# Kernel tuning notes

Measured on AMD Instinct MI355X. Metric: run time of the kernel, lower is better.

## Reference

```python
import jax, jax.numpy as jnp
import numpy as np

B = 4096          # batch size (per-view)
D = 128           # projection dim
TEMPERATURE = 0.5
TAU_PLUS = 0.1
DROP_FN = True


def setup_inputs() -> dict:
    key = jax.random.key(0)
    k1, k2, k3, k4 = jax.random.split(key, 4)

    def unit(k):
        x = jax.random.normal(k, (B, D), dtype=jnp.float32)
        return x / jnp.linalg.norm(x, axis=-1, keepdims=True)

    # contrastive embeddings are L2-normalized in practice (also keeps exp() in range)
    out_1 = unit(k1)
    out_2 = unit(k2)
    out_m = unit(k3)  # unused by the loss math, present in the signature
    target = jax.random.randint(k4, (B,), 0, 100, dtype=jnp.int32)
    return {"out_1": out_1, "out_2": out_2, "out_m": out_m, "target": target}


def reference(out_1, out_2, out_m, target):
    b = out_1.shape[0]
    n = 2 * b - 2
    out = jnp.concatenate([out_1, out_2], axis=0)          # [2B, D]
    sim = jnp.exp((out @ out.T) / TEMPERATURE)              # [2B, 2B]
    full = sim.sum(axis=-1)                                 # [2B]

    idx = jnp.arange(2 * b)
    # negative mask: exclude self and the paired augmentation (cols i, i+B for row i mod B)
    neg_mask = (idx[:, None] % b) != (idx[None, :] % b)     # [2B, 2B] bool
    keep = neg_mask
    if DROP_FN:
        t = jnp.concatenate([target, target], axis=0)       # [2B]
        # rows with target == -1 are never masked (broadcast over columns, as in torch)
        tmask = (t[:, None] == t[None, :]) & (t[:, None] != -1)
        keep = keep & jnp.logical_not(tmask)

    Ng = jnp.where(keep, sim, 0.0).sum(axis=-1)             # [2B]
    o1 = full - (1.0 - TAU_PLUS) * Ng
    o2 = full + (n * TAU_PLUS - (1.0 - TAU_PLUS)) * Ng
    loss = (-jnp.log(o1 / o2)).mean()
    return loss
```

## Files before the change

kernel.cpp:

```cpp
#include <hip/hip_runtime.h>
#include <hip/hip_bf16.h>

typedef __attribute__((ext_vector_type(8))) short bf16x8;
typedef __attribute__((ext_vector_type(4))) float f32x4;

constexpr int BQ  = 4096;
constexpr int DD  = 128;
constexpr int N2  = 2 * BQ;
constexpr int NCHK = 8;
constexpr int NCT  = 8;
constexpr float SQS = 1.6986433f;

static __device__ __forceinline__ ushort f2bf(float f) {
    unsigned u = __builtin_bit_cast(unsigned, f);
    u += 0x7FFFu + ((u >> 16) & 1u);
    return (ushort)(u >> 16);
}

__global__ __launch_bounds__(256) void convert_k(const float* __restrict__ a,
        const float* __restrict__ b, const int* __restrict__ tgt,
        ushort* __restrict__ obF, int* __restrict__ key)
{
    int t = blockIdx.x * 256 + threadIdx.x;
    int row = t >> 4, c8 = t & 15;
    const float* src = (row < BQ) ? (a + (size_t)row * DD + c8 * 8)
                                  : (b + (size_t)(row - BQ) * DD + c8 * 8);
    float4 v0 = reinterpret_cast<const float4*>(src)[0];
    float4 v1 = reinterpret_cast<const float4*>(src)[1];
    bf16x8 res;
    res[0] = (short)f2bf(v0.x * SQS); res[1] = (short)f2bf(v0.y * SQS);
    res[2] = (short)f2bf(v0.z * SQS); res[3] = (short)f2bf(v0.w * SQS);
    res[4] = (short)f2bf(v1.x * SQS); res[5] = (short)f2bf(v1.y * SQS);
    res[6] = (short)f2bf(v1.z * SQS); res[7] = (short)f2bf(v1.w * SQS);
    int frag = ((row >> 4) * 4 + (c8 >> 2)) * 64 + (c8 & 3) * 16 + (row & 15);
    *reinterpret_cast<bf16x8*>(obF + (size_t)frag * 8) = res;

    if (t < N2) {
        int tv = tgt[t & (BQ - 1)];
        key[t] = (tv == -1) ? (0x40000000 + (t & (BQ - 1))) : tv;
    }
}

__global__ __launch_bounds__(512, 4) void simloss_main(
        const ushort* __restrict__ obF, const int* __restrict__ key,
        float* __restrict__ pf, float* __restrict__ png)
{
    __shared__ float rred[2][128][2];

    const int tid  = threadIdx.x;
    const int lane = tid & 63;
    const int wid  = tid >> 6;
    const int wr   = wid >> 1;
    const int wc   = wid & 1;
    const int l15  = lane & 15;
    const int l4   = lane >> 4;

    const int raw = blockIdx.x;
    const int bid = (raw & 7) * 64 + (raw >> 3);
    const int ch  = bid >> 6;
    const int rt  = bid & 63;
    const int rowbase = rt * 128;

    const bf16x8* F = reinterpret_cast<const bf16x8*>(obF);

    bf16x8 af[2][4];
#pragma unroll
    for (int m = 0; m < 2; ++m)
#pragma unroll
        for (int kk = 0; kk < 4; ++kk)
            af[m][kk] = F[((rt * 8 + wr * 2 + m) * 4 + kk) * 64 + lane];

    int rk[2][4];
#pragma unroll
    for (int m = 0; m < 2; ++m)
#pragma unroll
        for (int r = 0; r < 4; ++r)
            rk[m][r] = key[rowbase + wr * 32 + m * 16 + l4 * 4 + r];

    float fs[2][4] = {}, ns[2][4] = {};

    const bf16x8* Bp = F + (size_t)(ch * 64 + wc * 4) * 4 * 64 + lane;
    const int*    kp = key + ch * 1024 + wc * 64 + l15;

#pragma unroll 1
    for (int ct = 0; ct < NCT; ++ct) {
        const bf16x8* Bct = Bp + ct * 2048;
        int ck[4];
#pragma unroll
        for (int n = 0; n < 4; ++n)
            ck[n] = kp[ct * 128 + n * 16];

        f32x4 acc[2][4] = {};
#pragma unroll
        for (int kk = 0; kk < 4; ++kk) {
            bf16x8 bf[4];
#pragma unroll
            for (int n = 0; n < 4; ++n)
                bf[n] = Bct[(n * 4 + kk) * 64];
#pragma unroll
            for (int m = 0; m < 2; ++m)
#pragma unroll
                for (int n = 0; n < 4; ++n)
                    acc[m][n] = __builtin_amdgcn_mfma_f32_16x16x32_bf16(
                        af[m][kk], bf[n], acc[m][n], 0, 0, 0);
        }

#pragma unroll
        for (int m = 0; m < 2; ++m)
#pragma unroll
            for (int n = 0; n < 4; ++n)
#pragma unroll
                for (int r = 0; r < 4; ++r) {
                    float e = __builtin_amdgcn_exp2f(acc[m][n][r]);
                    fs[m][r] += e;
                    ns[m][r] += (rk[m][r] == ck[n]) ? 0.0f : e;
                }
    }

#pragma unroll
    for (int m = 0; m < 2; ++m)
#pragma unroll
        for (int r = 0; r < 4; ++r) {
            float f = fs[m][r], g = ns[m][r];
#pragma unroll
            for (int msk = 1; msk < 16; msk <<= 1) {
                f += __shfl_xor(f, msk);
                g += __shfl_xor(g, msk);
            }
            if (l15 == 0) {
                int rl = wr * 32 + m * 16 + l4 * 4 + r;
                rred[wc][rl][0] = f;
                rred[wc][rl][1] = g;
            }
        }
    __syncthreads();
    if (tid < 128) {
        float f = rred[0][tid][0] + rred[1][tid][0];
        float g = rred[0][tid][1] + rred[1][tid][1];
        pf [ch * N2 + rowbase + tid] = f;
        png[ch * N2 + rowbase + tid] = g;
    }
}

__global__ __launch_bounds__(256) void row_loss_k(
        const float* __restrict__ pf, const float* __restrict__ png,
        float* __restrict__ bpart)
{
    int row = blockIdx.x * 256 + threadIdx.x;
    float full = 0.f, ng = 0.f;
#pragma unroll
    for (int s = 0; s < NCHK; ++s) {
        full += pf[s * N2 + row];
        ng   += png[s * N2 + row];
    }
    float o1 = full - 0.9f * ng;
    float o2 = full + 818.1f * ng;
    float li = (__builtin_amdgcn_logf(o2) - __builtin_amdgcn_logf(o1)) * 0.6931471805599453f;

#pragma unroll
    for (int m = 1; m < 64; m <<= 1) li += __shfl_xor(li, m);
    __shared__ float red[4];
    if ((threadIdx.x & 63) == 0) red[threadIdx.x >> 6] = li;
    __syncthreads();
    if (threadIdx.x == 0) bpart[blockIdx.x] = red[0] + red[1] + red[2] + red[3];
}

__global__ void final_k(const float* __restrict__ bpart, float* __restrict__ out)
{
    int l = threadIdx.x;
    float v = (l < 32) ? bpart[l] : 0.f;
#pragma unroll
    for (int m = 1; m < 32; m <<= 1) v += __shfl_xor(v, m);
    if (l == 0) out[0] = v / (float)N2;
}

extern "C" void kernel_launch(void* const* d_in, const int* in_sizes, int n_in,
                              void* d_out, int out_size, void* d_ws, size_t ws_size,
                              hipStream_t stream)
{
    const float* out1 = (const float*)d_in[0];
    const float* out2 = (const float*)d_in[1];
    const int*   tgt  = (const int*)d_in[3];
    float* out = (float*)d_out;

    ushort* obF  = (ushort*)d_ws;
    float*  pf   = (float*)((char*)d_ws + (2u << 20));
    float*  png  = (float*)((char*)d_ws + (2u << 20) + 262144);
    int*    key  = (int*)  ((char*)d_ws + (2u << 20) + 524288);
    float*  bpart= (float*)((char*)d_ws + (2u << 20) + 524288 + 32768);

    convert_k<<<(N2 * DD / 8) / 256, 256, 0, stream>>>(out1, out2, tgt, obF, key);
    simloss_main<<<512, 512, 0, stream>>>(obF, key, pf, png);
    row_loss_k<<<N2 / 256, 256, 0, stream>>>(pf, png, bpart);
    final_k<<<1, 64, 0, stream>>>(bpart, out);
}
```

Baseline: 39.94 us.

## Switch similarity GEMM to FP8 MFMA with register double-buffered B tiles

Embeddings are now converted to FP8 instead of bf16, which halves the operand footprint, and the similarity tiles use the fp8 16x16x32 MFMA. The main kernel moves to 256-thread blocks where each wave owns 64 rows and 32 columns per tile, and B fragments are double-buffered in registers so the next tile's loads overlap the current tile's compute. The intent is to cut memory traffic and raise MFMA throughput. The cost is a large precision loss in the exp'd logits, since the inputs are scaled by 1/(T*ln2)^0.5 before rounding to FP8, which may push the loss past tolerance.

```diff
diff --git a/kernel.cpp b/kernel.cpp
--- a/kernel.cpp
+++ b/kernel.cpp
@@ -1,25 +1,18 @@
 #include <hip/hip_runtime.h>
 #include <hip/hip_bf16.h>
 
-typedef __attribute__((ext_vector_type(8))) short bf16x8;
 typedef __attribute__((ext_vector_type(4))) float f32x4;
 
 constexpr int BQ  = 4096;
 constexpr int DD  = 128;
 constexpr int N2  = 2 * BQ;
 constexpr int NCHK = 8;
-constexpr int NCT  = 8;
+constexpr int NCT  = 16;
 constexpr float SQS = 1.6986433f;
-
-static __device__ __forceinline__ ushort f2bf(float f) {
-    unsigned u = __builtin_bit_cast(unsigned, f);
-    u += 0x7FFFu + ((u >> 16) & 1u);
-    return (ushort)(u >> 16);
-}
 
 __global__ __launch_bounds__(256) void convert_k(const float* __restrict__ a,
         const float* __restrict__ b, const int* __restrict__ tgt,
-        ushort* __restrict__ obF, int* __restrict__ key)
+        long* __restrict__ obF, int* __restrict__ key)
 {
     int t = blockIdx.x * 256 + threadIdx.x;
     int row = t >> 4, c8 = t & 15;
@@ -27,13 +20,13 @@
                                   : (b + (size_t)(row - BQ) * DD + c8 * 8);
     float4 v0 = reinterpret_cast<const float4*>(src)[0];
     float4 v1 = reinterpret_cast<const float4*>(src)[1];
-    bf16x8 res;
-    res[0] = (short)f2bf(v0.x * SQS); res[1] = (short)f2bf(v0.y * SQS);
-    res[2] = (short)f2bf(v0.z * SQS); res[3] = (short)f2bf(v0.w * SQS);
-    res[4] = (short)f2bf(v1.x * SQS); res[5] = (short)f2bf(v1.y * SQS);
-    res[6] = (short)f2bf(v1.z * SQS); res[7] = (short)f2bf(v1.w * SQS);
+    int lo = __builtin_amdgcn_cvt_pk_fp8_f32(v0.x * SQS, v0.y * SQS, 0, false);
+    lo     = __builtin_amdgcn_cvt_pk_fp8_f32(v0.z * SQS, v0.w * SQS, lo, true);
+    int hi = __builtin_amdgcn_cvt_pk_fp8_f32(v1.x * SQS, v1.y * SQS, 0, false);
+    hi     = __builtin_amdgcn_cvt_pk_fp8_f32(v1.z * SQS, v1.w * SQS, hi, true);
+    long v = (((long)hi) << 32) | (unsigned)lo;
     int frag = ((row >> 4) * 4 + (c8 >> 2)) * 64 + (c8 & 3) * 16 + (row & 15);
-    *reinterpret_cast<bf16x8*>(obF + (size_t)frag * 8) = res;
+    obF[frag] = v;
 
     if (t < N2) {
         int tv = tgt[t & (BQ - 1)];
@@ -41,8 +34,8 @@
     }
 }
 
-__global__ __launch_bounds__(512, 4) void simloss_main(
-        const ushort* __restrict__ obF, const int* __restrict__ key,
+__global__ __launch_bounds__(256, 3) void simloss_main(
+        const long* __restrict__ F8, const int* __restrict__ key,
         float* __restrict__ pf, float* __restrict__ png)
 {
     __shared__ float rred[2][128][2];
@@ -61,64 +54,67 @@
     const int rt  = bid & 63;
     const int rowbase = rt * 128;
 
-    const bf16x8* F = reinterpret_cast<const bf16x8*>(obF);
-
-    bf16x8 af[2][4];
+    long af[4][4];
 #pragma unroll
-    for (int m = 0; m < 2; ++m)
+    for (int m = 0; m < 4; ++m)
 #pragma unroll
         for (int kk = 0; kk < 4; ++kk)
-            af[m][kk] = F[((rt * 8 + wr * 2 + m) * 4 + kk) * 64 + lane];
+            af[m][kk] = F8[((rt * 8 + wr * 4 + m) * 4 + kk) * 64 + lane];
 
-    int rk[2][4];
+    int rk[4][4];
 #pragma unroll
-    for (int m = 0; m < 2; ++m)
+    for (int m = 0; m < 4; ++m)
 #pragma unroll
         for (int r = 0; r < 4; ++r)
-            rk[m][r] = key[rowbase + wr * 32 + m * 16 + l4 * 4 + r];
+            rk[m][r] = key[rowbase + wr * 64 + m * 16 + l4 * 4 + r];
 
-    float fs[2][4] = {}, ns[2][4] = {};
+    float fs[4][4] = {}, ns[4][4] = {};
 
-    const bf16x8* Bp = F + (size_t)(ch * 64 + wc * 4) * 4 * 64 + lane;
-    const int*    kp = key + ch * 1024 + wc * 64 + l15;
+    const long* Bw = F8 + (size_t)(ch * 256 + wc * 8) * 64 + lane;
+    const int*  kp = key + ch * 1024 + wc * 32 + l15;
 
+    auto loadB = [&](long bx[8], int ct) {
+        const long* p = Bw + ct * 1024;
+#pragma unroll
+        for (int q = 0; q < 8; ++q) bx[q] = p[q * 64];
+    };
+    auto compute = [&](const long bx[8], int ct) {
+        int ck0 = kp[ct * 64];
+        int ck1 = kp[ct * 64 + 16];
+        f32x4 acc[4][2] = {};
+#pragma unroll
+        for (int kk = 0; kk < 4; ++kk)
+#pragma unroll
+            for (int m = 0; m < 4; ++m) {
+                acc[m][0] = __builtin_amdgcn_mfma_f32_16x16x32_fp8_fp8(
+                    af[m][kk], bx[kk], acc[m][0], 0, 0, 0);
+                acc[m][1] = __builtin_amdgcn_mfma_f32_16x16x32_fp8_fp8(
+                    af[m][kk], bx[4 + kk], acc[m][1], 0, 0, 0);
+            }
+#pragma unroll
+        for (int m = 0; m < 4; ++m)
+#pragma unroll
+            for (int r = 0; r < 4; ++r) {
+                float e0 = __builtin_amdgcn_exp2f(acc[m][0][r]);
+                float e1 = __builtin_amdgcn_exp2f(acc[m][1][r]);
+                fs[m][r] += e0 + e1;
+                ns[m][r] += ((rk[m][r] == ck0) ? 0.0f : e0)
+                          + ((rk[m][r] == ck1) ? 0.0f : e1);
+            }
+    };
+
+    long bA[8], bB[8];
+    loadB(bA, 0);
 #pragma unroll 1
-    for (int ct = 0; ct < NCT; ++ct) {
-        const bf16x8* Bct = Bp + ct * 2048;
-        int ck[4];
-#pragma unroll
-        for (int n = 0; n < 4; ++n)
-            ck[n] = kp[ct * 128 + n * 16];
-
-        f32x4 acc[2][4] = {};
-#pragma unroll
-        for (int kk = 0; kk < 4; ++kk) {
-            bf16x8 bf[4];
-#pragma unroll
-            for (int n = 0; n < 4; ++n)
-                bf[n] = Bct[(n * 4 + kk) * 64];
-#pragma unroll
-            for (int m = 0; m < 2; ++m)
-#pragma unroll
-                for (int n = 0; n < 4; ++n)
-                    acc[m][n] = __builtin_amdgcn_mfma_f32_16x16x32_bf16(
-                        af[m][kk], bf[n], acc[m][n], 0, 0, 0);
-        }
-
-#pragma unroll
-        for (int m = 0; m < 2; ++m)
-#pragma unroll
-            for (int n = 0; n < 4; ++n)
-#pragma unroll
-                for (int r = 0; r < 4; ++r) {
-                    float e = __builtin_amdgcn_exp2f(acc[m][n][r]);
-                    fs[m][r] += e;
-                    ns[m][r] += (rk[m][r] == ck[n]) ? 0.0f : e;
-                }
+    for (int ct = 0; ct < NCT; ct += 2) {
+        loadB(bB, ct + 1);
+        compute(bA, ct);
+        if (ct + 2 < NCT) loadB(bA, ct + 2);
+        compute(bB, ct + 1);
     }
 
 #pragma unroll
-    for (int m = 0; m < 2; ++m)
+    for (int m = 0; m < 4; ++m)
 #pragma unroll
         for (int r = 0; r < 4; ++r) {
             float f = fs[m][r], g = ns[m][r];
@@ -128,17 +124,15 @@
                 g += __shfl_xor(g, msk);
             }
             if (l15 == 0) {
-                int rl = wr * 32 + m * 16 + l4 * 4 + r;
+                int rl = wr * 64 + m * 16 + l4 * 4 + r;
                 rred[wc][rl][0] = f;
                 rred[wc][rl][1] = g;
             }
         }
     __syncthreads();
     if (tid < 128) {
-        float f = rred[0][tid][0] + rred[1][tid][0];
-        float g = rred[0][tid][1] + rred[1][tid][1];
-        pf [ch * N2 + rowbase + tid] = f;
-        png[ch * N2 + rowbase + tid] = g;
+        pf [ch * N2 + rowbase + tid] = rred[0][tid][0] + rred[1][tid][0];
+        png[ch * N2 + rowbase + tid] = rred[0][tid][1] + rred[1][tid][1];
     }
 }
 
@@ -183,14 +177,14 @@
     const int*   tgt  = (const int*)d_in[3];
     float* out = (float*)d_out;
 
-    ushort* obF  = (ushort*)d_ws;
-    float*  pf   = (float*)((char*)d_ws + (2u << 20));
-    float*  png  = (float*)((char*)d_ws + (2u << 20) + 262144);
-    int*    key  = (int*)  ((char*)d_ws + (2u << 20) + 524288);
-    float*  bpart= (float*)((char*)d_ws + (2u << 20) + 524288 + 32768);
+    long*   obF  = (long*)d_ws;
+    float*  pf   = (float*)((char*)d_ws + (1u << 20));
+    float*  png  = (float*)((char*)d_ws + (1u << 20) + 262144);
+    int*    key  = (int*)  ((char*)d_ws + (1u << 20) + 524288);
+    float*  bpart= (float*)((char*)d_ws + (1u << 20) + 524288 + 32768);
 
-    convert_k<<<(N2 * DD / 8) / 256, 256, 0, stream>>>(out1, out2, tgt, obF, key);
-    simloss_main<<<512, 512, 0, stream>>>(obF, key, pf, png);
+    convert_k<<<512, 256, 0, stream>>>(out1, out2, tgt, obF, key);
+    simloss_main<<<512, 256, 0, stream>>>(obF, key, pf, png);
     row_loss_k<<<N2 / 256, 256, 0, stream>>>(pf, png, bpart);
     final_k<<<1, 64, 0, stream>>>(bpart, out);
 }
```

Result: faster. 38.36 us (-4.0%).
